# Performance work log

Hardware: AMD Instinct MI355X
Metric: run time of the kernel (lower is better)

The kernel has to match this reference:

```python
import jax, jax.numpy as jnp
import numpy as np

N_PIXELS = 262144  # 512x512 FOV
N_COMP = 1000      # neuron components (columns of sparse A)
NNZ = 400000       # ~400 nonzero pixels per component
N_BG = 2           # dense background columns
BATCH = 128


def setup_inputs() -> dict:
    key = jax.random.key(0)
    k0, k1, k2, k3, k4 = jax.random.split(key, 5)
    X = jax.random.normal(k0, (BATCH, N_PIXELS), dtype=jnp.float32)
    A_rows = jax.random.randint(k1, (NNZ,), 0, N_PIXELS, dtype=jnp.int32)
    A_cols = jax.random.randint(k2, (NNZ,), 0, N_COMP, dtype=jnp.int32)
    A_vals = jax.random.normal(k3, (NNZ,), dtype=jnp.float32)
    b = jax.random.normal(k4, (N_PIXELS, N_BG), dtype=jnp.float32)
    n_AtA = jnp.float32(1000.0)  # Frobenius norm of Ab.T @ Ab (constant scalar)
    return {"X": X, "A_vals": A_vals, "b": b, "n_AtA": n_AtA,
            "A_rows": A_rows, "A_cols": A_cols}


def reference(X, A_vals, b, n_AtA, A_rows, A_cols):
    # Sparse A^T @ X^T in COO form: gather pixel rows of X, scale by values,
    # segment-sum into component rows. data: [nnz, batch]
    data = X[:, A_rows].T * A_vals[:, None]
    Y = jax.ops.segment_sum(data, A_cols, num_segments=N_COMP)  # [n_comp, batch]
    # Dense background term: b^T @ X^T -> [n_bg, batch]
    Y1 = jnp.einsum('pg,bp->gb', b, X)
    Y = jnp.concatenate([Y, Y1], axis=0) / n_AtA
    return Y
```

## Files before the change

kernel.cpp:

```cpp
#include <hip/hip_runtime.h>
#include <hip/hip_bf16.h>

typedef unsigned short u16;
typedef unsigned int   u32;

#define N_PIXELS 262144
#define N_COMP   1000
#define NNZ      400000
#define N_BG     2
#define BATCH    128

#define CAP        576
#define TP_PIX     32
#define TS         36
#define TP_BLOCKS  (N_PIXELS / TP_PIX)
#define SC_NB      ((NNZ + 255) / 256)
#define QMAX       ((CAP + 3) / 4)
#define BG_BLOCKS  256
#define BG_PPB     (N_PIXELS / BG_BLOCKS)

#define CNT_PAD 16

#define WS_CNT    0
#define WS_SLOTS  65536
#define WS_XT     (WS_SLOTS + (size_t)N_COMP * CAP * 8)
#define WS_NEED   (WS_XT + (size_t)N_PIXELS * BATCH * 2)

__device__ __forceinline__ float bflo(u32 w) { return __uint_as_float(w << 16); }
__device__ __forceinline__ float bfhi(u32 w) { return __uint_as_float(w & 0xffff0000u); }


__global__ __launch_bounds__(256, 8) void pre_kernel(
    const float* __restrict__ X,
    const int*   __restrict__ rows, const int* __restrict__ cols,
    const float* __restrict__ vals, const float* __restrict__ nAtA,
    int* __restrict__ cnts, int2* __restrict__ slots,
    u32* __restrict__ XT32)
{
    __shared__ float smem[BATCH * TS];
    const int tid = threadIdx.x;

    if (blockIdx.x < SC_NB) {
        const int j = blockIdx.x * 256 + tid;
        if (j < NNZ) {
            const int c   = cols[j];
            const int pos = atomicAdd(&cnts[c * CNT_PAD], 1);
            if (pos < CAP) {
                int2 e;
                e.x = rows[j];
                e.y = __float_as_int(vals[j] * (1.0f / nAtA[0]));
                slots[(size_t)c * CAP + pos] = e;
            }
        }
    } else {
        const int p0 = (blockIdx.x - SC_NB) * TP_PIX;
        const int k  = tid & 7;
        const int bq = tid >> 3;
#pragma unroll
        for (int pass = 0; pass < 4; ++pass) {
            const int b = pass * 32 + bq;
            const float4 x = *(const float4*)(X + (size_t)b * N_PIXELS + p0 + 4 * k);
            const int m = (b >> 4) & 7;
            *(float4*)&smem[b * TS + 4 * (k ^ m)] = x;
        }
        __syncthreads();

        const int p    = tid >> 3;
        const int j0   = (tid & 7) * 16;
        const int m    = (j0 >> 4) & 7;
        const int slot = 4 * ((p >> 2) ^ m) + (p & 3);
        const float* col = smem + slot;
        u32 out[8];
#pragma unroll
        for (int q = 0; q < 8; ++q) {
            const float lo = col[(j0 + 2 * q)     * TS];
            const float hi = col[(j0 + 2 * q + 1) * TS];
            __hip_bfloat162 h2 = __float22bfloat162_rn(make_float2(lo, hi));
            u32 w; __builtin_memcpy(&w, &h2, 4);
            out[q] = w;
        }
        uint4* dst = (uint4*)(XT32 + (size_t)(p0 + p) * 64 + (j0 >> 1));
        dst[0] = make_uint4(out[0], out[1], out[2], out[3]);
        dst[1] = make_uint4(out[4], out[5], out[6], out[7]);
    }
}


__global__ __launch_bounds__(256) void compute_kernel(
    const uint4* __restrict__ XP4,
    const int*   __restrict__ cnts,
    const int2*  __restrict__ slots,
    const float* __restrict__ bmat,
    const float* __restrict__ nAtA,
    float* __restrict__ Y)
{
    __shared__ char smem_raw[12544];
    const int tid  = threadIdx.x;
    const int wave = tid >> 6;
    const int lane = tid & 63;
    const int g    = tid >> 4;
    const int s    = tid & 15;
    const int blk  = blockIdx.x;

    if (blk < 4 * N_COMP) {
        const int comp = blk >> 2;
        const int qr   = blk & 3;

        int*   sro = (int*)smem_raw;
        float* svv = (float*)(sro + QMAX);
        float* red = (float*)(svv + QMAX);

        int cnt = cnts[comp * CNT_PAD]; if (cnt > CAP) cnt = CAP;
        const int per = (cnt + 3) >> 2;
        const int beg = qr * per;
        int end = beg + per; if (end > cnt) end = cnt;
        const int n = (end > beg) ? (end - beg) : 0;
        const int n_pad = (n + 15) & ~15;

        const int2* sl = slots + (size_t)comp * CAP + beg;
        for (int i = tid; i < n_pad; i += 256) {
            int r = 0; float v = 0.0f;
            if (i < n) { const int2 e = sl[i]; r = e.x; v = __int_as_float(e.y); }
            sro[i] = r << 4;
            svv[i] = v;
        }
        __syncthreads();

        float acc[8] = {0, 0, 0, 0, 0, 0, 0, 0};
        int i = 0;
        for (; i + 32 <= n_pad; i += 32) {
            const int   e0 = i + g;
            const int   e1 = i + 16 + g;
            const int   r0 = sro[e0];
            const int   r1 = sro[e1];
            const float v0 = svv[e0];
            const float v1 = svv[e1];
            const uint4 x0 = XP4[r0 + s];
            const uint4 x1 = XP4[r1 + s];
            acc[0] += v0 * bflo(x0.x); acc[1] += v0 * bfhi(x0.x);
            acc[2] += v0 * bflo(x0.y); acc[3] += v0 * bfhi(x0.y);
            acc[4] += v0 * bflo(x0.z); acc[5] += v0 * bfhi(x0.z);
            acc[6] += v0 * bflo(x0.w); acc[7] += v0 * bfhi(x0.w);
            acc[0] += v1 * bflo(x1.x); acc[1] += v1 * bfhi(x1.x);
            acc[2] += v1 * bflo(x1.y); acc[3] += v1 * bfhi(x1.y);
            acc[4] += v1 * bflo(x1.z); acc[5] += v1 * bfhi(x1.z);
            acc[6] += v1 * bflo(x1.w); acc[7] += v1 * bfhi(x1.w);
        }
        for (; i < n_pad; i += 16) {
            const int   e = i + g;
            const float v = svv[e];
            const uint4 x = XP4[sro[e] + s];
            acc[0] += v * bflo(x.x); acc[1] += v * bfhi(x.x);
            acc[2] += v * bflo(x.y); acc[3] += v * bfhi(x.y);
            acc[4] += v * bflo(x.z); acc[5] += v * bfhi(x.z);
            acc[6] += v * bflo(x.w); acc[7] += v * bfhi(x.w);
        }
#pragma unroll
        for (int m = 16; m <= 32; m <<= 1)
#pragma unroll
            for (int q = 0; q < 8; ++q) acc[q] += __shfl_xor(acc[q], m, 64);
        if (lane < 16)
#pragma unroll
            for (int q = 0; q < 8; ++q) red[wave * 128 + lane * 8 + q] = acc[q];
        __syncthreads();
        if (tid < 128) {
            const float r0 = red[tid] + red[128 + tid] + red[256 + tid] + red[384 + tid];
            atomicAdd(&Y[(size_t)comp * BATCH + tid], r0);
        }
    } else {
        float2* bb   = (float2*)smem_raw;
        float*  red0 = (float*)(bb + BG_PPB);
        float*  red1 = red0 + 512;

        const int p0 = (blk - 4 * N_COMP) * BG_PPB;
        const float2* bm2 = (const float2*)bmat;
        for (int i = tid; i < BG_PPB; i += 256) bb[i] = bm2[p0 + i];
        __syncthreads();

        float a0[8] = {0,0,0,0,0,0,0,0}, a1[8] = {0,0,0,0,0,0,0,0};
#pragma unroll 2
        for (int i = g; i < BG_PPB; i += 16) {
            const uint4  x  = XP4[(size_t)(p0 + i) * 16 + s];
            const float2 b2 = bb[i];
            const float f0 = bflo(x.x), f1 = bfhi(x.x), f2 = bflo(x.y), f3 = bfhi(x.y);
            const float f4 = bflo(x.z), f5 = bfhi(x.z), f6 = bflo(x.w), f7 = bfhi(x.w);
            a0[0] += b2.x * f0; a0[1] += b2.x * f1; a0[2] += b2.x * f2; a0[3] += b2.x * f3;
            a0[4] += b2.x * f4; a0[5] += b2.x * f5; a0[6] += b2.x * f6; a0[7] += b2.x * f7;
            a1[0] += b2.y * f0; a1[1] += b2.y * f1; a1[2] += b2.y * f2; a1[3] += b2.y * f3;
            a1[4] += b2.y * f4; a1[5] += b2.y * f5; a1[6] += b2.y * f6; a1[7] += b2.y * f7;
        }
#pragma unroll
        for (int m = 16; m <= 32; m <<= 1)
#pragma unroll
            for (int q = 0; q < 8; ++q) {
                a0[q] += __shfl_xor(a0[q], m, 64);
                a1[q] += __shfl_xor(a1[q], m, 64);
            }
        if (lane < 16)
#pragma unroll
            for (int q = 0; q < 8; ++q) {
                red0[wave * 128 + lane * 8 + q] = a0[q];
                red1[wave * 128 + lane * 8 + q] = a1[q];
            }
        __syncthreads();
        if (tid < 128) {
            const float inv = 1.0f / nAtA[0];
            float* Ybg = Y + (size_t)N_COMP * BATCH;
            const float r0 = red0[tid] + red0[128 + tid] + red0[256 + tid] + red0[384 + tid];
            const float r1 = red1[tid] + red1[128 + tid] + red1[256 + tid] + red1[384 + tid];
            atomicAdd(&Ybg[tid],         r0 * inv);
            atomicAdd(&Ybg[BATCH + tid], r1 * inv);
        }
    }
}


#define NB          8
#define NNZ_CHUNKS  64
#define CHUNK_SZ    ((NNZ + NNZ_CHUNKS - 1) / NNZ_CHUNKS)

__global__ __launch_bounds__(256) void fb_hist_kernel(
    const float* __restrict__ X, const float* __restrict__ vals,
    const int* __restrict__ rows, const int* __restrict__ cols,
    const float* __restrict__ nAtA, float* __restrict__ Y)
{
    __shared__ float hist[NB * N_COMP];
    const int tid = threadIdx.x, chunk = blockIdx.x, b0 = blockIdx.y * NB;
    for (int i = tid; i < NB * N_COMP; i += 256) hist[i] = 0.0f;
    __syncthreads();
    const float inv = 1.0f / nAtA[0];
    const int e0 = chunk * CHUNK_SZ;
    const int e1 = (e0 + CHUNK_SZ < NNZ) ? (e0 + CHUNK_SZ) : NNZ;
    const float* Xb = X + (size_t)b0 * N_PIXELS;
    for (int j = e0 + tid; j < e1; j += 256) {
        const int r = rows[j], c = cols[j];
        const float v = vals[j] * inv;
        float x[NB];
#pragma unroll
        for (int k = 0; k < NB; ++k) x[k] = Xb[(size_t)k * N_PIXELS + r];
#pragma unroll
        for (int k = 0; k < NB; ++k) atomicAdd(&hist[k * N_COMP + c], v * x[k]);
    }
    __syncthreads();
    for (int i = tid; i < N_COMP * NB; i += 256) {
        const int c = i >> 3, k = i & 7;
        atomicAdd(&Y[(size_t)c * BATCH + b0 + k], hist[k * N_COMP + c]);
    }
}

__global__ __launch_bounds__(256) void fb_bg_kernel(
    const float* __restrict__ X, const float* __restrict__ bmat,
    const float* __restrict__ nAtA, float* __restrict__ Y)
{
    const int b = blockIdx.x, chunk = blockIdx.y, tid = threadIdx.x;
    const int p0 = chunk * (N_PIXELS / 8);
    const float4* X4 = (const float4*)(X + (size_t)b * N_PIXELS + p0);
    const float4* B4 = (const float4*)(bmat + (size_t)p0 * N_BG);
    float s0 = 0.0f, s1 = 0.0f;
    for (int i = tid; i < (N_PIXELS / 8) / 4; i += 256) {
        const float4 x = X4[i];
        const float4 g0 = B4[2 * i], g1 = B4[2 * i + 1];
        s0 += x.x * g0.x + x.y * g0.z + x.z * g1.x + x.w * g1.z;
        s1 += x.x * g0.y + x.y * g0.w + x.z * g1.y + x.w * g1.w;
    }
#pragma unroll
    for (int off = 32; off > 0; off >>= 1) {
        s0 += __shfl_down(s0, off, 64);
        s1 += __shfl_down(s1, off, 64);
    }
    if ((tid & 63) == 0) {
        const float inv = 1.0f / nAtA[0];
        atomicAdd(&Y[(size_t)N_COMP * BATCH + b],       s0 * inv);
        atomicAdd(&Y[(size_t)(N_COMP + 1) * BATCH + b], s1 * inv);
    }
}


extern "C" void kernel_launch(void* const* d_in, const int* in_sizes, int n_in,
                              void* d_out, int out_size, void* d_ws, size_t ws_size,
                              hipStream_t stream) {
    const float* X     = (const float*)d_in[0];
    const float* Avals = (const float*)d_in[1];
    const float* bmat  = (const float*)d_in[2];
    const float* nAtA  = (const float*)d_in[3];
    const int*   Arows = (const int*)d_in[4];
    const int*   Acols = (const int*)d_in[5];
    float*       Y     = (float*)d_out;

    if (ws_size >= WS_NEED) {
        char* ws = (char*)d_ws;
        int*  cnts  = (int*)(ws + WS_CNT);
        int2* slots = (int2*)(ws + WS_SLOTS);
        u32*  XT32  = (u32*)(ws + WS_XT);

        hipMemsetAsync(cnts, 0, 65536, stream);
        hipMemsetAsync(d_out, 0, (size_t)out_size * sizeof(float), stream);

        pre_kernel<<<SC_NB + TP_BLOCKS, 256, 0, stream>>>(
            X, Arows, Acols, Avals, nAtA, cnts, slots, XT32);
        compute_kernel<<<4 * N_COMP + BG_BLOCKS, 256, 0, stream>>>(
            (const uint4*)XT32, cnts, slots, bmat, nAtA, Y);
    } else {
        hipMemsetAsync(d_out, 0, (size_t)out_size * sizeof(float), stream);
        dim3 sgrid(NNZ_CHUNKS, BATCH / NB);
        fb_hist_kernel<<<sgrid, 256, 0, stream>>>(X, Avals, Arows, Acols, nAtA, Y);
        dim3 bgrid(BATCH, 8);
        fb_bg_kernel<<<bgrid, 256, 0, stream>>>(X, bmat, nAtA, Y);
    }
}
```

Before: 266.7 us.

## Widen transpose tile to 128 pixels with XOR-swizzled shared memory layout

The X-to-bf16 transpose part of pre_kernel now processes 128 pixels per block instead of 32. It uses an unpadded shared tile with an XOR swizzle on float4 columns, and each thread writes a contiguous 64-element half-row of output. This is meant to cut block count and per-block overhead and to make loads and stores longer and more coalesced. The trade-off is more shared memory per block (64KB), more registers per thread (32 output words), and dropping the occupancy hint, so occupancy falls.

New measurement: 271.1 us. Within noise of the previous version (+1.6%).

```diff
diff --git a/kernel.cpp b/kernel.cpp
--- a/kernel.cpp
+++ b/kernel.cpp
@@ -11,8 +11,7 @@
 #define BATCH    128
 
 #define CAP        576
-#define TP_PIX     32
-#define TS         36
+#define TP_PIX     128
 #define TP_BLOCKS  (N_PIXELS / TP_PIX)
 #define SC_NB      ((NNZ + 255) / 256)
 #define QMAX       ((CAP + 3) / 4)
@@ -30,14 +29,14 @@
 __device__ __forceinline__ float bfhi(u32 w) { return __uint_as_float(w & 0xffff0000u); }
 
 
-__global__ __launch_bounds__(256, 8) void pre_kernel(
+__global__ __launch_bounds__(256) void pre_kernel(
     const float* __restrict__ X,
     const int*   __restrict__ rows, const int* __restrict__ cols,
     const float* __restrict__ vals, const float* __restrict__ nAtA,
     int* __restrict__ cnts, int2* __restrict__ slots,
     u32* __restrict__ XT32)
 {
-    __shared__ float smem[BATCH * TS];
+    __shared__ float smem[BATCH * TP_PIX];
     const int tid = threadIdx.x;
 
     if (blockIdx.x < SC_NB) {
@@ -54,34 +53,42 @@
         }
     } else {
         const int p0 = (blockIdx.x - SC_NB) * TP_PIX;
-        const int k  = tid & 7;
-        const int bq = tid >> 3;
-#pragma unroll
-        for (int pass = 0; pass < 4; ++pass) {
-            const int b = pass * 32 + bq;
-            const float4 x = *(const float4*)(X + (size_t)b * N_PIXELS + p0 + 4 * k);
-            const int m = (b >> 4) & 7;
-            *(float4*)&smem[b * TS + 4 * (k ^ m)] = x;
-        }
-        __syncthreads();
-
-        const int p    = tid >> 3;
-        const int j0   = (tid & 7) * 16;
-        const int m    = (j0 >> 4) & 7;
-        const int slot = 4 * ((p >> 2) ^ m) + (p & 3);
-        const float* col = smem + slot;
-        u32 out[8];
-#pragma unroll
-        for (int q = 0; q < 8; ++q) {
-            const float lo = col[(j0 + 2 * q)     * TS];
-            const float hi = col[(j0 + 2 * q + 1) * TS];
+
+        const int br = tid >> 3;
+        const int c0 = tid & 7;
+#pragma unroll
+        for (int pr = 0; pr < 4; ++pr) {
+            const int b = pr * 32 + br;
+            const float* src = X + (size_t)b * N_PIXELS + p0;
+            float4* drow = (float4*)&smem[b * TP_PIX];
+#pragma unroll
+            for (int i = 0; i < 4; ++i) {
+                const int c = c0 + 8 * i;
+                const float4 x = *(const float4*)(src + 4 * c);
+                drow[c ^ (b & 7)] = x;
+            }
+        }
+        __syncthreads();
+
+        const int p  = tid >> 1;
+        const int h  = tid & 1;
+        const int pc = p >> 2;
+        const int pj = p & 3;
+        u32 out[32];
+#pragma unroll
+        for (int q = 0; q < 32; ++q) {
+            const int b0 = h * 64 + 2 * q;
+            const int b1 = b0 + 1;
+            const float lo = smem[b0 * TP_PIX + 4 * (pc ^ (b0 & 7)) + pj];
+            const float hi = smem[b1 * TP_PIX + 4 * (pc ^ (b1 & 7)) + pj];
             __hip_bfloat162 h2 = __float22bfloat162_rn(make_float2(lo, hi));
             u32 w; __builtin_memcpy(&w, &h2, 4);
             out[q] = w;
         }
-        uint4* dst = (uint4*)(XT32 + (size_t)(p0 + p) * 64 + (j0 >> 1));
-        dst[0] = make_uint4(out[0], out[1], out[2], out[3]);
-        dst[1] = make_uint4(out[4], out[5], out[6], out[7]);
+        uint4* dst = (uint4*)(XT32 + (size_t)(p0 + p) * 64 + h * 32);
+#pragma unroll
+        for (int q = 0; q < 8; ++q)
+            dst[q] = make_uint4(out[4 * q], out[4 * q + 1], out[4 * q + 2], out[4 * q + 3]);
     }
 }
 
```

## Bin nonzeros by pixel chunk and stream X once with LDS accumulation

Applied to the files above, without the earlier changes.

The old column-sorted gather over a bf16 transposed copy of X is replaced by two kernels. The first bins nonzeros into 512-pixel chunks, packing column and local row together. The second streams fp32 X coalesced per chunk into LDS and scatters products into a per-block LDS accumulator of components by 8 batches using shared atomics. It also fuses the dense background dot product into the same pass. This removes the transpose write and the random gathers, but adds many LDS and global atomics and uses large shared memory per block, which limits occupancy.

New measurement: 484.9 us. 1.82x slower.

```diff
diff --git a/kernel.cpp b/kernel.cpp
--- a/kernel.cpp
+++ b/kernel.cpp
@@ -10,207 +10,147 @@
 #define N_BG     2
 #define BATCH    128
 
-#define CAP        576
-#define TP_PIX     32
-#define TS         36
-#define TP_BLOCKS  (N_PIXELS / TP_PIX)
-#define SC_NB      ((NNZ + 255) / 256)
-#define QMAX       ((CAP + 3) / 4)
-#define BG_BLOCKS  256
-#define BG_PPB     (N_PIXELS / BG_BLOCKS)
+
+#define CHUNK_PX   512
+#define NBIN       (N_PIXELS / CHUNK_PX)
+#define BINCAP     1024
+#define BIN_NB     128
+#define BIN_CHUNK  ((NNZ + BIN_NB - 1) / BIN_NB)
+#define FB_RNG     32
+#define FB_BT      16
+#define CHUNKS_PER_RNG (NBIN / FB_RNG)
 
 #define CNT_PAD 16
 
-#define WS_CNT    0
-#define WS_SLOTS  65536
-#define WS_XT     (WS_SLOTS + (size_t)N_COMP * CAP * 8)
-#define WS_NEED   (WS_XT + (size_t)N_PIXELS * BATCH * 2)
-
-__device__ __forceinline__ float bflo(u32 w) { return __uint_as_float(w << 16); }
-__device__ __forceinline__ float bfhi(u32 w) { return __uint_as_float(w & 0xffff0000u); }
-
-
-__global__ __launch_bounds__(256, 8) void pre_kernel(
-    const float* __restrict__ X,
+#define WS_BCNT   0
+#define WS_BSLOT  32768
+#define WS_NEED   (WS_BSLOT + (size_t)NBIN * BINCAP * 8)
+
+
+__global__ __launch_bounds__(256) void bin_kernel(
     const int*   __restrict__ rows, const int* __restrict__ cols,
     const float* __restrict__ vals, const float* __restrict__ nAtA,
-    int* __restrict__ cnts, int2* __restrict__ slots,
-    u32* __restrict__ XT32)
-{
-    __shared__ float smem[BATCH * TS];
+    int* __restrict__ bcnt, int2* __restrict__ bslot)
+{
+    __shared__ int hist[NBIN];
+    __shared__ int base[NBIN];
     const int tid = threadIdx.x;
 
-    if (blockIdx.x < SC_NB) {
-        const int j = blockIdx.x * 256 + tid;
-        if (j < NNZ) {
-            const int c   = cols[j];
-            const int pos = atomicAdd(&cnts[c * CNT_PAD], 1);
-            if (pos < CAP) {
-                int2 e;
-                e.x = rows[j];
-                e.y = __float_as_int(vals[j] * (1.0f / nAtA[0]));
-                slots[(size_t)c * CAP + pos] = e;
+    for (int i = tid; i < NBIN; i += 256) hist[i] = 0;
+    __syncthreads();
+
+    const int e0 = blockIdx.x * BIN_CHUNK;
+    const int e1 = (e0 + BIN_CHUNK < NNZ) ? (e0 + BIN_CHUNK) : NNZ;
+
+    for (int j = e0 + tid; j < e1; j += 256)
+        atomicAdd(&hist[rows[j] >> 9], 1);
+    __syncthreads();
+
+    for (int i = tid; i < NBIN; i += 256) {
+        const int h = hist[i];
+        base[i] = h ? atomicAdd(&bcnt[i * CNT_PAD], h) : 0;
+        hist[i] = 0;
+    }
+    __syncthreads();
+
+    const float inv = 1.0f / nAtA[0];
+    for (int j = e0 + tid; j < e1; j += 256) {
+        const int r   = rows[j];
+        const int bin = r >> 9;
+        const int pos = base[bin] + atomicAdd(&hist[bin], 1);
+        if (pos < BINCAP) {
+            int2 e;
+            e.x = (cols[j] << 9) | (r & 511);
+            e.y = __float_as_int(vals[j] * inv);
+            bslot[(size_t)bin * BINCAP + pos] = e;
+        }
+    }
+}
+
+
+__global__ __launch_bounds__(256) void fused_kernel(
+    const float* __restrict__ X,
+    const float* __restrict__ bmat,
+    const float* __restrict__ nAtA,
+    const int*   __restrict__ bcnt,
+    const int2*  __restrict__ bslot,
+    float* __restrict__ Y)
+{
+    __shared__ float xs[CHUNK_PX * 9];
+    __shared__ float acc[N_COMP * 9];
+    __shared__ int2  ent[BINCAP];
+
+    const int tid  = threadIdx.x;
+    const int rng  = blockIdx.x >> 4;
+    const int bt   = blockIdx.x & 15;
+    const int b0   = bt * 8;
+    const int bq   = tid >> 5;
+    const int qq   = tid & 31;
+    const int wave = tid >> 6;
+    const int lane = tid & 63;
+    const int sub  = lane >> 3;
+    const int bb   = lane & 7;
+
+    for (int i = tid; i < N_COMP * 9; i += 256) acc[i] = 0.0f;
+
+    const float*  xrow = X + (size_t)(b0 + bq) * N_PIXELS;
+    const float4* bm4  = (const float4*)bmat;
+    float bg0 = 0.0f, bg1 = 0.0f;
+
+    for (int cc = 0; cc < CHUNKS_PER_RNG; ++cc) {
+        const int bin = rng * CHUNKS_PER_RNG + cc;
+        const int p0  = bin * CHUNK_PX;
+        int nb = bcnt[bin * CNT_PAD]; if (nb > BINCAP) nb = BINCAP;
+
+        __syncthreads();
+
+        float4 t4[4];
+#pragma unroll
+        for (int i = 0; i < 4; ++i)
+            t4[i] = *(const float4*)(xrow + p0 + 4 * (qq + 32 * i));
+#pragma unroll
+        for (int i = 0; i < 4; ++i) {
+            const int pb = 4 * (qq + 32 * i);
+            const float* tf = (const float*)&t4[i];
+#pragma unroll
+            for (int j = 0; j < 4; ++j)
+                xs[(pb + j) * 9 + bq] = tf[j];
+#pragma unroll
+            for (int jj = 0; jj < 2; ++jj) {
+                const float4 g = bm4[(p0 + pb) / 2 + jj];
+                bg0 += g.x * tf[2 * jj]     + g.z * tf[2 * jj + 1];
+                bg1 += g.y * tf[2 * jj]     + g.w * tf[2 * jj + 1];
             }
         }
-    } else {
-        const int p0 = (blockIdx.x - SC_NB) * TP_PIX;
-        const int k  = tid & 7;
-        const int bq = tid >> 3;
-#pragma unroll
-        for (int pass = 0; pass < 4; ++pass) {
-            const int b = pass * 32 + bq;
-            const float4 x = *(const float4*)(X + (size_t)b * N_PIXELS + p0 + 4 * k);
-            const int m = (b >> 4) & 7;
-            *(float4*)&smem[b * TS + 4 * (k ^ m)] = x;
+        for (int i = tid; i < nb; i += 256)
+            ent[i] = bslot[(size_t)bin * BINCAP + i];
+        __syncthreads();
+
+        for (int e = wave * 8 + sub; e < nb; e += 32) {
+            const int2  en = ent[e];
+            const float v  = __int_as_float(en.y);
+            const int   rl = en.x & 511;
+            const int   c  = en.x >> 9;
+            atomicAdd(&acc[c * 9 + bb], v * xs[rl * 9 + bb]);
         }
-        __syncthreads();
-
-        const int p    = tid >> 3;
-        const int j0   = (tid & 7) * 16;
-        const int m    = (j0 >> 4) & 7;
-        const int slot = 4 * ((p >> 2) ^ m) + (p & 3);
-        const float* col = smem + slot;
-        u32 out[8];
-#pragma unroll
-        for (int q = 0; q < 8; ++q) {
-            const float lo = col[(j0 + 2 * q)     * TS];
-            const float hi = col[(j0 + 2 * q + 1) * TS];
-            __hip_bfloat162 h2 = __float22bfloat162_rn(make_float2(lo, hi));
-            u32 w; __builtin_memcpy(&w, &h2, 4);
-            out[q] = w;
-        }
-        uint4* dst = (uint4*)(XT32 + (size_t)(p0 + p) * 64 + (j0 >> 1));
-        dst[0] = make_uint4(out[0], out[1], out[2], out[3]);
-        dst[1] = make_uint4(out[4], out[5], out[6], out[7]);
-    }
-}
-
-
-__global__ __launch_bounds__(256) void compute_kernel(
-    const uint4* __restrict__ XP4,
-    const int*   __restrict__ cnts,
-    const int2*  __restrict__ slots,
-    const float* __restrict__ bmat,
-    const float* __restrict__ nAtA,
-    float* __restrict__ Y)
-{
-    __shared__ char smem_raw[12544];
-    const int tid  = threadIdx.x;
-    const int wave = tid >> 6;
-    const int lane = tid & 63;
-    const int g    = tid >> 4;
-    const int s    = tid & 15;
-    const int blk  = blockIdx.x;
-
-    if (blk < 4 * N_COMP) {
-        const int comp = blk >> 2;
-        const int qr   = blk & 3;
-
-        int*   sro = (int*)smem_raw;
-        float* svv = (float*)(sro + QMAX);
-        float* red = (float*)(svv + QMAX);
-
-        int cnt = cnts[comp * CNT_PAD]; if (cnt > CAP) cnt = CAP;
-        const int per = (cnt + 3) >> 2;
-        const int beg = qr * per;
-        int end = beg + per; if (end > cnt) end = cnt;
-        const int n = (end > beg) ? (end - beg) : 0;
-        const int n_pad = (n + 15) & ~15;
-
-        const int2* sl = slots + (size_t)comp * CAP + beg;
-        for (int i = tid; i < n_pad; i += 256) {
-            int r = 0; float v = 0.0f;
-            if (i < n) { const int2 e = sl[i]; r = e.x; v = __int_as_float(e.y); }
-            sro[i] = r << 4;
-            svv[i] = v;
-        }
-        __syncthreads();
-
-        float acc[8] = {0, 0, 0, 0, 0, 0, 0, 0};
-        int i = 0;
-        for (; i + 32 <= n_pad; i += 32) {
-            const int   e0 = i + g;
-            const int   e1 = i + 16 + g;
-            const int   r0 = sro[e0];
-            const int   r1 = sro[e1];
-            const float v0 = svv[e0];
-            const float v1 = svv[e1];
-            const uint4 x0 = XP4[r0 + s];
-            const uint4 x1 = XP4[r1 + s];
-            acc[0] += v0 * bflo(x0.x); acc[1] += v0 * bfhi(x0.x);
-            acc[2] += v0 * bflo(x0.y); acc[3] += v0 * bfhi(x0.y);
-            acc[4] += v0 * bflo(x0.z); acc[5] += v0 * bfhi(x0.z);
-            acc[6] += v0 * bflo(x0.w); acc[7] += v0 * bfhi(x0.w);
-            acc[0] += v1 * bflo(x1.x); acc[1] += v1 * bfhi(x1.x);
-            acc[2] += v1 * bflo(x1.y); acc[3] += v1 * bfhi(x1.y);
-            acc[4] += v1 * bflo(x1.z); acc[5] += v1 * bfhi(x1.z);
-            acc[6] += v1 * bflo(x1.w); acc[7] += v1 * bfhi(x1.w);
-        }
-        for (; i < n_pad; i += 16) {
-            const int   e = i + g;
-            const float v = svv[e];
-            const uint4 x = XP4[sro[e] + s];
-            acc[0] += v * bflo(x.x); acc[1] += v * bfhi(x.x);
-            acc[2] += v * bflo(x.y); acc[3] += v * bfhi(x.y);
-            acc[4] += v * bflo(x.z); acc[5] += v * bfhi(x.z);
-            acc[6] += v * bflo(x.w); acc[7] += v * bfhi(x.w);
-        }
-#pragma unroll
-        for (int m = 16; m <= 32; m <<= 1)
-#pragma unroll
-            for (int q = 0; q < 8; ++q) acc[q] += __shfl_xor(acc[q], m, 64);
-        if (lane < 16)
-#pragma unroll
-            for (int q = 0; q < 8; ++q) red[wave * 128 + lane * 8 + q] = acc[q];
-        __syncthreads();
-        if (tid < 128) {
-            const float r0 = red[tid] + red[128 + tid] + red[256 + tid] + red[384 + tid];
-            atomicAdd(&Y[(size_t)comp * BATCH + tid], r0);
-        }
-    } else {
-        float2* bb   = (float2*)smem_raw;
-        float*  red0 = (float*)(bb + BG_PPB);
-        float*  red1 = red0 + 512;
-
-        const int p0 = (blk - 4 * N_COMP) * BG_PPB;
-        const float2* bm2 = (const float2*)bmat;
-        for (int i = tid; i < BG_PPB; i += 256) bb[i] = bm2[p0 + i];
-        __syncthreads();
-
-        float a0[8] = {0,0,0,0,0,0,0,0}, a1[8] = {0,0,0,0,0,0,0,0};
-#pragma unroll 2
-        for (int i = g; i < BG_PPB; i += 16) {
-            const uint4  x  = XP4[(size_t)(p0 + i) * 16 + s];
-            const float2 b2 = bb[i];
-            const float f0 = bflo(x.x), f1 = bfhi(x.x), f2 = bflo(x.y), f3 = bfhi(x.y);
-            const float f4 = bflo(x.z), f5 = bfhi(x.z), f6 = bflo(x.w), f7 = bfhi(x.w);
-            a0[0] += b2.x * f0; a0[1] += b2.x * f1; a0[2] += b2.x * f2; a0[3] += b2.x * f3;
-            a0[4] += b2.x * f4; a0[5] += b2.x * f5; a0[6] += b2.x * f6; a0[7] += b2.x * f7;
-            a1[0] += b2.y * f0; a1[1] += b2.y * f1; a1[2] += b2.y * f2; a1[3] += b2.y * f3;
-            a1[4] += b2.y * f4; a1[5] += b2.y * f5; a1[6] += b2.y * f6; a1[7] += b2.y * f7;
-        }
-#pragma unroll
-        for (int m = 16; m <= 32; m <<= 1)
-#pragma unroll
-            for (int q = 0; q < 8; ++q) {
-                a0[q] += __shfl_xor(a0[q], m, 64);
-                a1[q] += __shfl_xor(a1[q], m, 64);
-            }
-        if (lane < 16)
-#pragma unroll
-            for (int q = 0; q < 8; ++q) {
-                red0[wave * 128 + lane * 8 + q] = a0[q];
-                red1[wave * 128 + lane * 8 + q] = a1[q];
-            }
-        __syncthreads();
-        if (tid < 128) {
-            const float inv = 1.0f / nAtA[0];
-            float* Ybg = Y + (size_t)N_COMP * BATCH;
-            const float r0 = red0[tid] + red0[128 + tid] + red0[256 + tid] + red0[384 + tid];
-            const float r1 = red1[tid] + red1[128 + tid] + red1[256 + tid] + red1[384 + tid];
-            atomicAdd(&Ybg[tid],         r0 * inv);
-            atomicAdd(&Ybg[BATCH + tid], r1 * inv);
-        }
+    }
+    __syncthreads();
+
+    for (int i = tid; i < N_COMP * 8; i += 256) {
+        const int c = i >> 3, b = i & 7;
+        const float a = acc[c * 9 + b];
+        if (a != 0.0f) atomicAdd(&Y[(size_t)c * BATCH + b0 + b], a);
+    }
+#pragma unroll
+    for (int off = 16; off; off >>= 1) {
+        bg0 += __shfl_down(bg0, off, 32);
+        bg1 += __shfl_down(bg1, off, 32);
+    }
+    if ((lane & 31) == 0) {
+        const float inv = 1.0f / nAtA[0];
+        float* Ybg = Y + (size_t)N_COMP * BATCH;
+        atomicAdd(&Ybg[b0 + bq],         bg0 * inv);
+        atomicAdd(&Ybg[BATCH + b0 + bq], bg1 * inv);
     }
 }
 
@@ -289,17 +229,16 @@
 
     if (ws_size >= WS_NEED) {
         char* ws = (char*)d_ws;
-        int*  cnts  = (int*)(ws + WS_CNT);
-        int2* slots = (int2*)(ws + WS_SLOTS);
-        u32*  XT32  = (u32*)(ws + WS_XT);
-
-        hipMemsetAsync(cnts, 0, 65536, stream);
+        int*  bcnt  = (int*)(ws + WS_BCNT);
+        int2* bslot = (int2*)(ws + WS_BSLOT);
+
+        hipMemsetAsync(bcnt, 0, NBIN * CNT_PAD * sizeof(int), stream);
         hipMemsetAsync(d_out, 0, (size_t)out_size * sizeof(float), stream);
 
-        pre_kernel<<<SC_NB + TP_BLOCKS, 256, 0, stream>>>(
-            X, Arows, Acols, Avals, nAtA, cnts, slots, XT32);
-        compute_kernel<<<4 * N_COMP + BG_BLOCKS, 256, 0, stream>>>(
-            (const uint4*)XT32, cnts, slots, bmat, nAtA, Y);
+        bin_kernel<<<BIN_NB, 256, 0, stream>>>(
+            Arows, Acols, Avals, nAtA, bcnt, bslot);
+        fused_kernel<<<FB_RNG * FB_BT, 256, 0, stream>>>(
+            X, bmat, nAtA, bcnt, bslot, Y);
     } else {
         hipMemsetAsync(d_out, 0, (size_t)out_size * sizeof(float), stream);
         dim3 sgrid(NNZ_CHUNKS, BATCH / NB);
```
